# Optimization experiments

Hardware: AMD Instinct MI355X
Metric: run time of the kernel (lower is better)

## Reference

```python
import jax, jax.numpy as jnp
import numpy as np

B, T, N, D = 2, 10, 1024, 1024
NH = 16
HD = D // NH


def setup_inputs() -> dict:
    key = jax.random.key(0)
    ks = jax.random.split(key, 9)
    data = jax.random.normal(ks[0], (B, N, D), jnp.float32)
    traj_pos = jax.random.normal(ks[1], (B, T, N, 3), jnp.float32)
    q = jax.random.normal(ks[2], (B, T, N, 4), jnp.float32)
    traj_quat = q / (jnp.linalg.norm(q, axis=-1, keepdims=True) + 1e-10)
    certainty = jax.random.uniform(ks[3], (B, N), jnp.float32)
    s = 1.0 / np.sqrt(D).astype(np.float32)
    Wq = jax.random.normal(ks[4], (D, D), jnp.float32) * s
    Wk = jax.random.normal(ks[5], (D, D), jnp.float32) * s
    Wv = jax.random.normal(ks[6], (D, D), jnp.float32) * s
    Wo = jax.random.normal(ks[7], (D, D), jnp.float32) * s
    z = jnp.zeros((D,), jnp.float32)
    return {"data": data, "traj_pos": traj_pos, "traj_quat": traj_quat,
            "certainty": certainty, "Wq": Wq, "bq": z, "Wk": Wk, "bk": z,
            "Wv": Wv, "bv": z, "Wo": Wo, "bo": z}


def reference(data, traj_pos, traj_quat, certainty, Wq, bq, Wk, bk, Wv, bv, Wo, bo):
    b, n, d = data.shape
    # --- trajectory similarity scores (same for all batches: torch.mean over batch+time) ---
    # pos_dist[i,j] = mean_{b,t} ||p_bti - p_btj||
    pd = jnp.linalg.norm(traj_pos[:, :, :, None, :] - traj_pos[:, :, None, :, :], axis=-1).mean(axis=(0, 1))  # (n,n)
    qdm = jnp.linalg.norm(traj_quat[:, :, :, None, :] - traj_quat[:, :, None, :, :], axis=-1).mean(axis=(0, 1))
    qdp = jnp.linalg.norm(traj_quat[:, :, :, None, :] + traj_quat[:, :, None, :, :], axis=-1).mean(axis=(0, 1))
    qd = jnp.minimum(qdm, qdp)
    traj = jnp.exp(-pd - qd)
    traj = traj / traj.sum(axis=-1, keepdims=True)  # (n,n) row-normalized

    def proj(x, W, bias):
        return (x @ W.T + bias).reshape(b, n, NH, HD).transpose(0, 2, 1, 3)  # (b,h,n,hd)

    Q = proj(data, Wq, bq)
    K = proj(data, Wk, bk)
    V = proj(data, Wv, bv)
    scores = jnp.einsum('bhid,bhjd->bhij', Q, K) / np.sqrt(HD).astype(np.float32)
    combined = scores + 0.5 * traj[None, None]  # broadcast over (batch, heads)
    attn = jax.nn.softmax(combined, axis=-1)
    out = jnp.einsum('bhij,bhjd->bhid', attn, V).transpose(0, 2, 1, 3).reshape(b, n, d)
    out = out @ Wo.T + bo
    # certainty update from attention entropy
    avg_attn = attn.mean(axis=1)  # (b,n,n)
    p = jnp.clip(avg_attn, 1e-10, None)
    Hent = -jnp.sum(p * jnp.log(p), axis=-1)  # (b,n)
    H_max = np.log(n).astype(np.float32)
    new_certainty = jnp.maximum(certainty, jax.nn.sigmoid(H_max - Hent))
    return out, new_certainty
```

## Files before the change

kernel.cpp:

```cpp
#include <hip/hip_runtime.h>
#include <math.h>

#define NB 2
#define NN 1024
#define DD 1024
#define NHH 16
#define HDD 64
#define BTT 20

typedef unsigned short u16;
typedef short bf16x8 __attribute__((ext_vector_type(8)));
typedef float f32x4 __attribute__((ext_vector_type(4)));

#define HMAXL 6.93147180559945f
#define C1 0.18033688011112042f
#define TLC 0.72134752044448170f
#define KC  0.072134752044448170f

#define TRAJ_OFF 0
#define TL_OFF    1048576
#define DATAB_OFF 1572864
#define WQB_OFF   2621440
#define WKB_OFF   3145728
#define WVB_OFF   3670016
#define WOB_OFF   4194304
#define QB_OFF    4718592
#define KB_OFF    5767168
#define VT_OFF    6815744
#define AOB_OFF   7864320
#define LV_OFF    8912896
#define HACC_OFF  8945664
#define RS_OFF    8947712

__device__ __forceinline__ float b2f(u16 h) { return __uint_as_float(((unsigned)h) << 16); }
__device__ __forceinline__ u16 f2bf(float f) {
  unsigned u = __float_as_uint(f);
  return (u16)((u + 0x7fffu + ((u >> 16) & 1u)) >> 16);
}
__device__ __forceinline__ void dma16(const void* g, void* l) {
  __builtin_amdgcn_global_load_lds((const __attribute__((address_space(1))) void*)g,
                                   (__attribute__((address_space(3))) void*)l, 16, 0, 0);
}

__global__ __launch_bounds__(256) void conv_data_kernel(const float* __restrict__ src,
                                                        u16* __restrict__ dst) {
  int i = (blockIdx.x * 256 + threadIdx.x) * 4;
  float4 v = *(const float4*)(src + i);
  ushort4 o = {f2bf(v.x), f2bf(v.y), f2bf(v.z), f2bf(v.w)};
  *(ushort4*)(dst + i) = o;
}

__global__ __launch_bounds__(256) void conv_w_kernel(const float* __restrict__ w0,
                                                     const float* __restrict__ w1,
                                                     const float* __restrict__ w2,
                                                     const float* __restrict__ w3,
                                                     u16* __restrict__ d0, u16* __restrict__ d1,
                                                     u16* __restrict__ d2, u16* __restrict__ d3) {
  int z = blockIdx.y;
  const float* s = z == 0 ? w0 : (z == 1 ? w1 : (z == 2 ? w2 : w3));
  u16* d = z == 0 ? d0 : (z == 1 ? d1 : (z == 2 ? d2 : d3));
  int i = (blockIdx.x * 256 + threadIdx.x) * 4;
  float4 v = *(const float4*)(s + i);
  ushort4 o = {f2bf(v.x), f2bf(v.y), f2bf(v.z), f2bf(v.w)};
  *(ushort4*)(d + i) = o;
}

__global__ __launch_bounds__(256) void trajA_kernel(const float* __restrict__ pos,
                                                    const float* __restrict__ quat,
                                                    float* __restrict__ w,
                                                    float* __restrict__ rs) {
  const int tid = threadIdx.x;
  const int j = blockIdx.x * 256 + tid;
  const int i0 = blockIdx.y * 8;
  __shared__ float ld[8][BTT][8];
  if (tid < 8 * BTT) {
    int ii = tid / BTT, bt = tid % BTT;
    const float* pp = pos + ((size_t)bt * NN + i0 + ii) * 3;
    ld[ii][bt][0] = pp[0]; ld[ii][bt][1] = pp[1]; ld[ii][bt][2] = pp[2];
    *(float4*)&ld[ii][bt][4] = *(const float4*)(quat + ((size_t)bt * NN + i0 + ii) * 4);
  }
  __syncthreads();
  float acc[8] = {};
  for (int bt = 0; bt < BTT; ++bt) {
    const float* pj = pos + ((size_t)bt * NN + j) * 3;
    float pjx = pj[0], pjy = pj[1], pjz = pj[2];
    float4 qj = *(const float4*)(quat + ((size_t)bt * NN + j) * 4);
#pragma unroll
    for (int ii = 0; ii < 8; ++ii) {
      float4 pi = *(const float4*)&ld[ii][bt][0];
      float4 qi = *(const float4*)&ld[ii][bt][4];
      float dx = pi.x - pjx, dy = pi.y - pjy, dz = pi.z - pjz;
      float d2 = fmaf(dz, dz, fmaf(dy, dy, dx * dx));
      float dot = fmaf(qi.w, qj.w, fmaf(qi.z, qj.z, fmaf(qi.y, qj.y, qi.x * qj.x)));
      float t = fmaf(-2.f, fabsf(dot), 2.f);
      acc[ii] += sqrtf(d2) + sqrtf(fmaxf(t, 0.f));
    }
  }
#pragma unroll
  for (int ii = 0; ii < 8; ++ii) {
    float v = exp2f(-acc[ii] * KC);
    w[(size_t)(i0 + ii) * NN + j] = v;
    float s = v;
#pragma unroll
    for (int off = 1; off < 64; off <<= 1) s += __shfl_xor(s, off, 64);
    if ((tid & 63) == 0) atomicAdd(&rs[i0 + ii], s);
  }
}

__global__ __launch_bounds__(256) void trajB_kernel(const float* __restrict__ w,
                                                    const float* __restrict__ rs,
                                                    u16* __restrict__ tl) {
  const int i = blockIdx.x;
  const int tid = threadIdx.x;
  float inv = TLC / rs[i];
  float4 w4 = *(const float4*)(w + (size_t)i * NN + tid * 4);
  ushort4 o = {f2bf(w4.x * inv), f2bf(w4.y * inv), f2bf(w4.z * inv), f2bf(w4.w * inv)};
  *(ushort4*)(tl + (size_t)i * NN + tid * 4) = o;
}

__global__ __launch_bounds__(256) void gemm_qkv_kernel(const u16* __restrict__ Ab,
                                                       const u16* __restrict__ Wq,
                                                       const u16* __restrict__ Wk,
                                                       const u16* __restrict__ Wv,
                                                       const float* __restrict__ bq,
                                                       const float* __restrict__ bk,
                                                       const float* __restrict__ bv,
                                                       u16* __restrict__ Qb,
                                                       u16* __restrict__ Kb,
                                                       u16* __restrict__ VtT) {
  const int z = blockIdx.z;
  const u16* Wb = z == 0 ? Wq : (z == 1 ? Wk : Wv);
  const float* bias = z == 0 ? bq : (z == 1 ? bk : bv);
  __shared__ __align__(16) u16 As[128 * 32];
  __shared__ __align__(16) u16 Ws[64 * 32];
  const int tid = threadIdx.x;
  const int w = tid >> 6, l = tid & 63, g = l >> 4, ln = l & 15;
  const int bm = blockIdx.y << 7, bn = blockIdx.x << 6;
  const int rowA0 = w * 32 + (l >> 2), rowA1 = rowA0 + 16;
  const int colA = (l & 3) * 8;
  const int rowB = w * 16 + (l >> 2);
  const u16* Aptr0 = Ab + (size_t)(bm + rowA0) * DD + colA;
  const u16* Aptr1 = Ab + (size_t)(bm + rowA1) * DD + colA;
  const u16* Bptr = Wb + (size_t)(bn + rowB) * DD + colA;
  u16* ldsA0 = As + (w * 2) * 512;
  u16* ldsA1 = As + (w * 2 + 1) * 512;
  u16* ldsB = Ws + w * 512;
  f32x4 zero4 = {0.f, 0.f, 0.f, 0.f};
  f32x4 acc[4][2];
#pragma unroll
  for (int mt = 0; mt < 4; ++mt) { acc[mt][0] = zero4; acc[mt][1] = zero4; }
  const int mlo = (w & 1) * 64, nlo = (w >> 1) * 32;
  for (int k0 = 0; k0 < DD; k0 += 32) {
    __syncthreads();
    dma16(Aptr0 + k0, ldsA0);
    dma16(Aptr1 + k0, ldsA1);
    dma16(Bptr + k0, ldsB);
    __syncthreads();
    bf16x8 bfr[2];
#pragma unroll
    for (int nt = 0; nt < 2; ++nt)
      bfr[nt] = *(const bf16x8*)&Ws[(nlo + nt * 16 + ln) * 32 + g * 8];
#pragma unroll
    for (int mt = 0; mt < 4; ++mt) {
      bf16x8 af = *(const bf16x8*)&As[(mlo + mt * 16 + ln) * 32 + g * 8];
#pragma unroll
      for (int nt = 0; nt < 2; ++nt)
        acc[mt][nt] = __builtin_amdgcn_mfma_f32_16x16x32_bf16(af, bfr[nt], acc[mt][nt], 0, 0, 0);
    }
  }
#pragma unroll
  for (int nt = 0; nt < 2; ++nt) {
    int n = bn + nlo + nt * 16 + ln;
    float bb = bias[n];
    if (z == 2) {
      int row = (((bm >> 10) << 4) + (n >> 6)) * 64 + (n & 63);
#pragma unroll
      for (int mt = 0; mt < 4; ++mt) {
        int tok = ((bm & 1023) + mlo + mt * 16 + g * 4);
        ushort4 pk = {f2bf(acc[mt][nt][0] + bb), f2bf(acc[mt][nt][1] + bb),
                      f2bf(acc[mt][nt][2] + bb), f2bf(acc[mt][nt][3] + bb)};
        *(ushort4*)(VtT + (size_t)row * NN + tok) = pk;
      }
    } else {
      u16* outp = z == 0 ? Qb : Kb;
#pragma unroll
      for (int mt = 0; mt < 4; ++mt) {
#pragma unroll
        for (int r = 0; r < 4; ++r) {
          int m = bm + mlo + mt * 16 + g * 4 + r;
          outp[(size_t)m * DD + n] = f2bf(acc[mt][nt][r] + bb);
        }
      }
    }
  }
}

__global__ __launch_bounds__(256) void gemm_o_kernel(const u16* __restrict__ Ab,
                                                     const u16* __restrict__ Wb,
                                                     const float* __restrict__ bias,
                                                     float* __restrict__ C) {
  __shared__ __align__(16) u16 As[128 * 32];
  __shared__ __align__(16) u16 Ws[64 * 32];
  const int tid = threadIdx.x;
  const int w = tid >> 6, l = tid & 63, g = l >> 4, ln = l & 15;
  const int bm = blockIdx.y << 7, bn = blockIdx.x << 6;
  const int rowA0 = w * 32 + (l >> 2), rowA1 = rowA0 + 16;
  const int colA = (l & 3) * 8;
  const int rowB = w * 16 + (l >> 2);
  const u16* Aptr0 = Ab + (size_t)(bm + rowA0) * DD + colA;
  const u16* Aptr1 = Ab + (size_t)(bm + rowA1) * DD + colA;
  const u16* Bptr = Wb + (size_t)(bn + rowB) * DD + colA;
  u16* ldsA0 = As + (w * 2) * 512;
  u16* ldsA1 = As + (w * 2 + 1) * 512;
  u16* ldsB = Ws + w * 512;
  f32x4 zero4 = {0.f, 0.f, 0.f, 0.f};
  f32x4 acc[4][2];
#pragma unroll
  for (int mt = 0; mt < 4; ++mt) { acc[mt][0] = zero4; acc[mt][1] = zero4; }
  const int mlo = (w & 1) * 64, nlo = (w >> 1) * 32;
  for (int k0 = 0; k0 < DD; k0 += 32) {
    __syncthreads();
    dma16(Aptr0 + k0, ldsA0);
    dma16(Aptr1 + k0, ldsA1);
    dma16(Bptr + k0, ldsB);
    __syncthreads();
    bf16x8 bfr[2];
#pragma unroll
    for (int nt = 0; nt < 2; ++nt)
      bfr[nt] = *(const bf16x8*)&Ws[(nlo + nt * 16 + ln) * 32 + g * 8];
#pragma unroll
    for (int mt = 0; mt < 4; ++mt) {
      bf16x8 af = *(const bf16x8*)&As[(mlo + mt * 16 + ln) * 32 + g * 8];
#pragma unroll
      for (int nt = 0; nt < 2; ++nt)
        acc[mt][nt] = __builtin_amdgcn_mfma_f32_16x16x32_bf16(af, bfr[nt], acc[mt][nt], 0, 0, 0);
    }
  }
#pragma unroll
  for (int nt = 0; nt < 2; ++nt) {
    int n = bn + nlo + nt * 16 + ln;
    float bb = bias[n];
#pragma unroll
    for (int mt = 0; mt < 4; ++mt) {
#pragma unroll
      for (int r = 0; r < 4; ++r) {
        int m = bm + mlo + mt * 16 + g * 4 + r;
        C[(size_t)m * DD + n] = acc[mt][nt][r] + bb;
      }
    }
  }
}

__global__ __launch_bounds__(256) void att_kernel(const u16* __restrict__ Qb,
                                                  const u16* __restrict__ Kb,
                                                  const u16* __restrict__ VtT,
                                                  const u16* __restrict__ tl,
                                                  u16* __restrict__ AOb,
                                                  float* __restrict__ Lv) {
  const int tid = threadIdx.x;
  const int bh = blockIdx.y;
  const int b = bh >> 4, h = bh & 15;
  const int i0 = blockIdx.x << 6;
  const int w = tid >> 6, l = tid & 63, g = l >> 4, ln = l & 15;
  const int wi0 = w * 16;
  __shared__ __align__(16) u16 Qs[64 * 64];
  __shared__ __align__(16) u16 Ks[64 * 64];
  __shared__ __align__(16) u16 Vts[64 * 64];
  __shared__ __align__(16) u16 Pt[64 * 72];
  __shared__ float lsc[64];
  const int drow0 = w * 16 + (l >> 3), drow1 = drow0 + 8;
  const int dcol = (l & 7) * 8;
  dma16(Qb + ((size_t)(b * NN) + i0 + drow0) * DD + h * HDD + dcol, Qs + (w * 2) * 512);
  dma16(Qb + ((size_t)(b * NN) + i0 + drow1) * DD + h * HDD + dcol, Qs + (w * 2 + 1) * 512);
  const int ig = i0 + wi0 + ln;
  f32x4 zero4 = {0.f, 0.f, 0.f, 0.f};
  f32x4 oacc[4];
#pragma unroll
  for (int nt = 0; nt < 4; ++nt) oacc[nt] = zero4;
  float lacc = 0.f;
  for (int j0 = 0; j0 < NN; j0 += 64) {
    __syncthreads();
    dma16(Kb + ((size_t)(b * NN) + j0 + drow0) * DD + h * HDD + dcol, Ks + (w * 2) * 512);
    dma16(Kb + ((size_t)(b * NN) + j0 + drow1) * DD + h * HDD + dcol, Ks + (w * 2 + 1) * 512);
    dma16(VtT + ((size_t)(bh * 64) + drow0) * NN + j0 + dcol, Vts + (w * 2) * 512);
    dma16(VtT + ((size_t)(bh * 64) + drow1) * NN + j0 + dcol, Vts + (w * 2 + 1) * 512);
    ushort4 tlv[4];
#pragma unroll
    for (int jt = 0; jt < 4; ++jt)
      tlv[jt] = *(const ushort4*)(tl + (size_t)ig * NN + j0 + jt * 16 + g * 4);
    __syncthreads();
    bf16x8 qf[2];
    qf[0] = *(const bf16x8*)&Qs[(wi0 + ln) * 64 + g * 8];
    qf[1] = *(const bf16x8*)&Qs[(wi0 + ln) * 64 + 32 + g * 8];
    f32x4 sacc[4];
#pragma unroll
    for (int jt = 0; jt < 4; ++jt) {
      sacc[jt] = zero4;
#pragma unroll
      for (int kc = 0; kc < 2; ++kc) {
        bf16x8 af = *(const bf16x8*)&Ks[(jt * 16 + ln) * 64 + kc * 32 + g * 8];
        sacc[jt] = __builtin_amdgcn_mfma_f32_16x16x32_bf16(af, qf[kc], sacc[jt], 0, 0, 0);
      }
    }
#pragma unroll
    for (int jt = 0; jt < 4; ++jt) {
      float e0 = exp2f(sacc[jt][0] * C1 + b2f(tlv[jt].x));
      float e1 = exp2f(sacc[jt][1] * C1 + b2f(tlv[jt].y));
      float e2 = exp2f(sacc[jt][2] * C1 + b2f(tlv[jt].z));
      float e3 = exp2f(sacc[jt][3] * C1 + b2f(tlv[jt].w));
      lacc += (e0 + e1) + (e2 + e3);
      ushort4 pk = {f2bf(e0), f2bf(e1), f2bf(e2), f2bf(e3)};
      *(ushort4*)(Pt + (wi0 + ln) * 72 + jt * 16 + g * 4) = pk;
    }
    __syncthreads();
    bf16x8 pf[2];
    pf[0] = *(const bf16x8*)&Pt[(wi0 + ln) * 72 + g * 8];
    pf[1] = *(const bf16x8*)&Pt[(wi0 + ln) * 72 + 32 + g * 8];
#pragma unroll
    for (int nt = 0; nt < 4; ++nt) {
#pragma unroll
      for (int kc = 0; kc < 2; ++kc) {
        bf16x8 vf = *(const bf16x8*)&Vts[(nt * 16 + ln) * 64 + kc * 32 + g * 8];
        oacc[nt] = __builtin_amdgcn_mfma_f32_16x16x32_bf16(pf[kc], vf, oacc[nt], 0, 0, 0);
      }
    }
  }
  lacc += __shfl_xor(lacc, 16, 64);
  lacc += __shfl_xor(lacc, 32, 64);
  if (g == 0) {
    Lv[(size_t)bh * NN + i0 + wi0 + ln] = lacc;
    lsc[wi0 + ln] = 1.f / lacc;
  }
  __syncthreads();
#pragma unroll
  for (int nt = 0; nt < 4; ++nt) {
    int d = nt * 16 + ln;
#pragma unroll
    for (int r = 0; r < 4; ++r) {
      int i = wi0 + g * 4 + r;
      float v = oacc[nt][r] * lsc[i];
      AOb[((size_t)(b * NN) + i0 + i) * DD + h * HDD + d] = f2bf(v);
    }
  }
}

__global__ __launch_bounds__(256) void ent_kernel(const u16* __restrict__ Qb,
                                                  const u16* __restrict__ Kb,
                                                  const u16* __restrict__ tl,
                                                  const float* __restrict__ Lv,
                                                  float* __restrict__ Hacc) {
  const int tid = threadIdx.x;
  const int j0 = blockIdx.x << 6;
  const int i0 = blockIdx.y << 6;
  const int b = blockIdx.z;
  const int w = tid >> 6, l = tid & 63, g = l >> 4, ln = l & 15;
  const int wi0 = w * 16;
  __shared__ __align__(16) u16 Qs[64 * 64];
  __shared__ __align__(16) u16 Ks[64 * 64];
  __shared__ float linv[NHH][64];
#pragma unroll
  for (int rep = 0; rep < 4; ++rep) {
    int idx = tid + (rep << 8);
    int hh = idx >> 6, ii = idx & 63;
    linv[hh][ii] = 1.f / Lv[((size_t)((b << 4) + hh)) * NN + i0 + ii];
  }
  const int drow0 = w * 16 + (l >> 3), drow1 = drow0 + 8;
  const int dcol = (l & 7) * 8;
  const int ig = i0 + wi0 + ln;
  ushort4 tlv[4];
#pragma unroll
  for (int jt = 0; jt < 4; ++jt)
    tlv[jt] = *(const ushort4*)(tl + (size_t)ig * NN + j0 + jt * 16 + g * 4);
  float P[4][4] = {};
  f32x4 zero4 = {0.f, 0.f, 0.f, 0.f};
  for (int h = 0; h < NHH; ++h) {
    __syncthreads();
    dma16(Qb + ((size_t)(b * NN) + i0 + drow0) * DD + h * HDD + dcol, Qs + (w * 2) * 512);
    dma16(Qb + ((size_t)(b * NN) + i0 + drow1) * DD + h * HDD + dcol, Qs + (w * 2 + 1) * 512);
    dma16(Kb + ((size_t)(b * NN) + j0 + drow0) * DD + h * HDD + dcol, Ks + (w * 2) * 512);
    dma16(Kb + ((size_t)(b * NN) + j0 + drow1) * DD + h * HDD + dcol, Ks + (w * 2 + 1) * 512);
    __syncthreads();
    float li = linv[h][wi0 + ln];
    bf16x8 qf[2];
    qf[0] = *(const bf16x8*)&Qs[(wi0 + ln) * 64 + g * 8];
    qf[1] = *(const bf16x8*)&Qs[(wi0 + ln) * 64 + 32 + g * 8];
#pragma unroll
    for (int jt = 0; jt < 4; ++jt) {
      f32x4 sacc = zero4;
#pragma unroll
      for (int kc = 0; kc < 2; ++kc) {
        bf16x8 af = *(const bf16x8*)&Ks[(jt * 16 + ln) * 64 + kc * 32 + g * 8];
        sacc = __builtin_amdgcn_mfma_f32_16x16x32_bf16(af, qf[kc], sacc, 0, 0, 0);
      }
      P[jt][0] += exp2f(sacc[0] * C1 + b2f(tlv[jt].x)) * li;
      P[jt][1] += exp2f(sacc[1] * C1 + b2f(tlv[jt].y)) * li;
      P[jt][2] += exp2f(sacc[2] * C1 + b2f(tlv[jt].z)) * li;
      P[jt][3] += exp2f(sacc[3] * C1 + b2f(tlv[jt].w)) * li;
    }
  }
  float hs = 0.f;
#pragma unroll
  for (int jt = 0; jt < 4; ++jt) {
#pragma unroll
    for (int r = 0; r < 4; ++r) {
      float p = fmaxf(P[jt][r] * (1.f / NHH), 1e-10f);
      hs -= p * logf(p);
    }
  }
  hs += __shfl_xor(hs, 16, 64);
  hs += __shfl_xor(hs, 32, 64);
  if (g == 0) atomicAdd(&Hacc[(size_t)b * NN + i0 + wi0 + ln], hs);
}

__global__ __launch_bounds__(256) void zero_acc_kernel(float* __restrict__ p) {
  p[blockIdx.x * 256 + threadIdx.x] = 0.f;
}

__global__ __launch_bounds__(256) void cert_kernel(const float* __restrict__ Hacc,
                                                   const float* __restrict__ cert,
                                                   float* __restrict__ outc) {
  int idx = blockIdx.x * 256 + threadIdx.x;
  float H = Hacc[idx];
  float sg = 1.f / (1.f + expf(H - HMAXL));
  outc[idx] = fmaxf(cert[idx], sg);
}

extern "C" void kernel_launch(void* const* d_in, const int* in_sizes, int n_in,
                              void* d_out, int out_size, void* d_ws, size_t ws_size,
                              hipStream_t stream) {
  const float* data      = (const float*)d_in[0];
  const float* traj_pos  = (const float*)d_in[1];
  const float* traj_quat = (const float*)d_in[2];
  const float* certainty = (const float*)d_in[3];
  const float* Wq = (const float*)d_in[4];
  const float* bq = (const float*)d_in[5];
  const float* Wk = (const float*)d_in[6];
  const float* bk = (const float*)d_in[7];
  const float* Wv = (const float*)d_in[8];
  const float* bv = (const float*)d_in[9];
  const float* Wo = (const float*)d_in[10];
  const float* bo = (const float*)d_in[11];

  float* ws = (float*)d_ws;
  float* wtr  = ws + TRAJ_OFF;
  u16* tl    = (u16*)(ws + TL_OFF);
  u16* datab = (u16*)(ws + DATAB_OFF);
  u16* wqb   = (u16*)(ws + WQB_OFF);
  u16* wkb   = (u16*)(ws + WKB_OFF);
  u16* wvb   = (u16*)(ws + WVB_OFF);
  u16* wob   = (u16*)(ws + WOB_OFF);
  u16* Qb    = (u16*)(ws + QB_OFF);
  u16* Kb    = (u16*)(ws + KB_OFF);
  u16* VtT   = (u16*)(ws + VT_OFF);
  u16* AOb   = (u16*)(ws + AOB_OFF);
  float* Lv   = ws + LV_OFF;
  float* Hacc = ws + HACC_OFF;
  float* rs   = ws + RS_OFF;
  float* out  = (float*)d_out;
  float* outc = out + (size_t)NB * NN * DD;

  zero_acc_kernel<<<12, 256, 0, stream>>>(Hacc);
  conv_data_kernel<<<2048, 256, 0, stream>>>(data, datab);
  conv_w_kernel<<<dim3(1024, 4), 256, 0, stream>>>(Wq, Wk, Wv, Wo, wqb, wkb, wvb, wob);
  trajA_kernel<<<dim3(4, 128), 256, 0, stream>>>(traj_pos, traj_quat, wtr, rs);
  trajB_kernel<<<NN, 256, 0, stream>>>(wtr, rs, tl);
  gemm_qkv_kernel<<<dim3(16, 16, 3), 256, 0, stream>>>(datab, wqb, wkb, wvb, bq, bk, bv,
                                                       Qb, Kb, VtT);
  att_kernel<<<dim3(NN / 64, NB * NHH), 256, 0, stream>>>(Qb, Kb, VtT, tl, AOb, Lv);
  ent_kernel<<<dim3(NN / 64, NN / 64, NB), 256, 0, stream>>>(Qb, Kb, tl, Lv, Hacc);
  cert_kernel<<<(NB * NN) / 256, 256, 0, stream>>>(Hacc, certainty, outc);
  gemm_o_kernel<<<dim3(16, 16), 256, 0, stream>>>(AOb, wob, bo, out);
}
```

Before: 232.2 us.

## Enlarge GEMM tiles, batch attention/entropy key loads, merge conversion kernels

```diff
diff --git a/kernel.cpp b/kernel.cpp
--- a/kernel.cpp
+++ b/kernel.cpp
@@ -42,24 +42,24 @@
                                    (__attribute__((address_space(3))) void*)l, 16, 0, 0);
 }
 
-__global__ __launch_bounds__(256) void conv_data_kernel(const float* __restrict__ src,
-                                                        u16* __restrict__ dst) {
-  int i = (blockIdx.x * 256 + threadIdx.x) * 4;
-  float4 v = *(const float4*)(src + i);
-  ushort4 o = {f2bf(v.x), f2bf(v.y), f2bf(v.z), f2bf(v.w)};
-  *(ushort4*)(dst + i) = o;
-}
-
-__global__ __launch_bounds__(256) void conv_w_kernel(const float* __restrict__ w0,
-                                                     const float* __restrict__ w1,
-                                                     const float* __restrict__ w2,
-                                                     const float* __restrict__ w3,
-                                                     u16* __restrict__ d0, u16* __restrict__ d1,
-                                                     u16* __restrict__ d2, u16* __restrict__ d3) {
+__global__ __launch_bounds__(256) void conv_kernel(const float* __restrict__ data,
+                                                   const float* __restrict__ w0,
+                                                   const float* __restrict__ w1,
+                                                   const float* __restrict__ w2,
+                                                   const float* __restrict__ w3,
+                                                   u16* __restrict__ dd,
+                                                   u16* __restrict__ d0, u16* __restrict__ d1,
+                                                   u16* __restrict__ d2, u16* __restrict__ d3) {
   int z = blockIdx.y;
-  const float* s = z == 0 ? w0 : (z == 1 ? w1 : (z == 2 ? w2 : w3));
-  u16* d = z == 0 ? d0 : (z == 1 ? d1 : (z == 2 ? d2 : d3));
-  int i = (blockIdx.x * 256 + threadIdx.x) * 4;
+  const float* s;
+  u16* d;
+  size_t off = 0;
+  if (z < 2) { s = data; d = dd; off = (size_t)z * 1048576; }
+  else if (z == 2) { s = w0; d = d0; }
+  else if (z == 3) { s = w1; d = d1; }
+  else if (z == 4) { s = w2; d = d2; }
+  else { s = w3; d = d3; }
+  size_t i = off + (size_t)(blockIdx.x * 256 + threadIdx.x) * 4;
   float4 v = *(const float4*)(s + i);
   ushort4 o = {f2bf(v.x), f2bf(v.y), f2bf(v.z), f2bf(v.w)};
   *(ushort4*)(d + i) = o;
@@ -132,51 +132,54 @@
   const u16* Wb = z == 0 ? Wq : (z == 1 ? Wk : Wv);
   const float* bias = z == 0 ? bq : (z == 1 ? bk : bv);
   __shared__ __align__(16) u16 As[128 * 32];
-  __shared__ __align__(16) u16 Ws[64 * 32];
+  __shared__ __align__(16) u16 Bs[128 * 32];
   const int tid = threadIdx.x;
   const int w = tid >> 6, l = tid & 63, g = l >> 4, ln = l & 15;
-  const int bm = blockIdx.y << 7, bn = blockIdx.x << 6;
-  const int rowA0 = w * 32 + (l >> 2), rowA1 = rowA0 + 16;
-  const int colA = (l & 3) * 8;
-  const int rowB = w * 16 + (l >> 2);
-  const u16* Aptr0 = Ab + (size_t)(bm + rowA0) * DD + colA;
-  const u16* Aptr1 = Ab + (size_t)(bm + rowA1) * DD + colA;
-  const u16* Bptr = Wb + (size_t)(bn + rowB) * DD + colA;
-  u16* ldsA0 = As + (w * 2) * 512;
-  u16* ldsA1 = As + (w * 2 + 1) * 512;
-  u16* ldsB = Ws + w * 512;
+  const int bm = blockIdx.y << 7, bn = blockIdx.x << 7;
+  const int srow = w * 16 + (l >> 2);
+  const int scol = (l & 3) * 8;
+  const u16* Ap0 = Ab + (size_t)(bm + srow) * DD + scol;
+  const u16* Ap1 = Ab + (size_t)(bm + 64 + srow) * DD + scol;
+  const u16* Bp0 = Wb + (size_t)(bn + srow) * DD + scol;
+  const u16* Bp1 = Wb + (size_t)(bn + 64 + srow) * DD + scol;
+  u16* dA0 = As + w * 512;
+  u16* dA1 = As + 2048 + w * 512;
+  u16* dB0 = Bs + w * 512;
+  u16* dB1 = Bs + 2048 + w * 512;
+  const int mw = (w & 1) * 64, nw = (w >> 1) * 64;
   f32x4 zero4 = {0.f, 0.f, 0.f, 0.f};
-  f32x4 acc[4][2];
-#pragma unroll
-  for (int mt = 0; mt < 4; ++mt) { acc[mt][0] = zero4; acc[mt][1] = zero4; }
-  const int mlo = (w & 1) * 64, nlo = (w >> 1) * 32;
+  f32x4 acc[4][4];
+#pragma unroll
+  for (int mt = 0; mt < 4; ++mt)
+#pragma unroll
+    for (int nt = 0; nt < 4; ++nt) acc[mt][nt] = zero4;
   for (int k0 = 0; k0 < DD; k0 += 32) {
     __syncthreads();
-    dma16(Aptr0 + k0, ldsA0);
-    dma16(Aptr1 + k0, ldsA1);
-    dma16(Bptr + k0, ldsB);
-    __syncthreads();
-    bf16x8 bfr[2];
-#pragma unroll
-    for (int nt = 0; nt < 2; ++nt)
-      bfr[nt] = *(const bf16x8*)&Ws[(nlo + nt * 16 + ln) * 32 + g * 8];
-#pragma unroll
-    for (int mt = 0; mt < 4; ++mt) {
-      bf16x8 af = *(const bf16x8*)&As[(mlo + mt * 16 + ln) * 32 + g * 8];
-#pragma unroll
-      for (int nt = 0; nt < 2; ++nt)
-        acc[mt][nt] = __builtin_amdgcn_mfma_f32_16x16x32_bf16(af, bfr[nt], acc[mt][nt], 0, 0, 0);
-    }
-  }
-#pragma unroll
-  for (int nt = 0; nt < 2; ++nt) {
-    int n = bn + nlo + nt * 16 + ln;
+    dma16(Ap0 + k0, dA0); dma16(Ap1 + k0, dA1);
+    dma16(Bp0 + k0, dB0); dma16(Bp1 + k0, dB1);
+    __syncthreads();
+    bf16x8 bfr[4], afr[4];
+#pragma unroll
+    for (int nt = 0; nt < 4; ++nt)
+      bfr[nt] = *(const bf16x8*)&Bs[(nw + nt * 16 + ln) * 32 + g * 8];
+#pragma unroll
+    for (int mt = 0; mt < 4; ++mt)
+      afr[mt] = *(const bf16x8*)&As[(mw + mt * 16 + ln) * 32 + g * 8];
+#pragma unroll
+    for (int mt = 0; mt < 4; ++mt)
+#pragma unroll
+      for (int nt = 0; nt < 4; ++nt)
+        acc[mt][nt] = __builtin_amdgcn_mfma_f32_16x16x32_bf16(afr[mt], bfr[nt], acc[mt][nt], 0, 0, 0);
+  }
+#pragma unroll
+  for (int nt = 0; nt < 4; ++nt) {
+    int n = bn + nw + nt * 16 + ln;
     float bb = bias[n];
     if (z == 2) {
       int row = (((bm >> 10) << 4) + (n >> 6)) * 64 + (n & 63);
 #pragma unroll
       for (int mt = 0; mt < 4; ++mt) {
-        int tok = ((bm & 1023) + mlo + mt * 16 + g * 4);
+        int tok = (bm & 1023) + mw + mt * 16 + g * 4;
         ushort4 pk = {f2bf(acc[mt][nt][0] + bb), f2bf(acc[mt][nt][1] + bb),
                       f2bf(acc[mt][nt][2] + bb), f2bf(acc[mt][nt][3] + bb)};
         *(ushort4*)(VtT + (size_t)row * NN + tok) = pk;
@@ -187,7 +190,7 @@
       for (int mt = 0; mt < 4; ++mt) {
 #pragma unroll
         for (int r = 0; r < 4; ++r) {
-          int m = bm + mlo + mt * 16 + g * 4 + r;
+          int m = bm + mw + mt * 16 + g * 4 + r;
           outp[(size_t)m * DD + n] = f2bf(acc[mt][nt][r] + bb);
         }
       }
@@ -200,51 +203,54 @@
                                                      const float* __restrict__ bias,
                                                      float* __restrict__ C) {
   __shared__ __align__(16) u16 As[128 * 32];
-  __shared__ __align__(16) u16 Ws[64 * 32];
+  __shared__ __align__(16) u16 Bs[128 * 32];
   const int tid = threadIdx.x;
   const int w = tid >> 6, l = tid & 63, g = l >> 4, ln = l & 15;
-  const int bm = blockIdx.y << 7, bn = blockIdx.x << 6;
-  const int rowA0 = w * 32 + (l >> 2), rowA1 = rowA0 + 16;
-  const int colA = (l & 3) * 8;
-  const int rowB = w * 16 + (l >> 2);
-  const u16* Aptr0 = Ab + (size_t)(bm + rowA0) * DD + colA;
-  const u16* Aptr1 = Ab + (size_t)(bm + rowA1) * DD + colA;
-  const u16* Bptr = Wb + (size_t)(bn + rowB) * DD + colA;
-  u16* ldsA0 = As + (w * 2) * 512;
-  u16* ldsA1 = As + (w * 2 + 1) * 512;
-  u16* ldsB = Ws + w * 512;
+  const int bm = blockIdx.y << 7, bn = blockIdx.x << 7;
+  const int srow = w * 16 + (l >> 2);
+  const int scol = (l & 3) * 8;
+  const u16* Ap0 = Ab + (size_t)(bm + srow) * DD + scol;
+  const u16* Ap1 = Ab + (size_t)(bm + 64 + srow) * DD + scol;
+  const u16* Bp0 = Wb + (size_t)(bn + srow) * DD + scol;
+  const u16* Bp1 = Wb + (size_t)(bn + 64 + srow) * DD + scol;
+  u16* dA0 = As + w * 512;
+  u16* dA1 = As + 2048 + w * 512;
+  u16* dB0 = Bs + w * 512;
+  u16* dB1 = Bs + 2048 + w * 512;
+  const int mw = (w & 1) * 64, nw = (w >> 1) * 64;
   f32x4 zero4 = {0.f, 0.f, 0.f, 0.f};
-  f32x4 acc[4][2];
-#pragma unroll
-  for (int mt = 0; mt < 4; ++mt) { acc[mt][0] = zero4; acc[mt][1] = zero4; }
-  const int mlo = (w & 1) * 64, nlo = (w >> 1) * 32;
+  f32x4 acc[4][4];
+#pragma unroll
+  for (int mt = 0; mt < 4; ++mt)
+#pragma unroll
+    for (int nt = 0; nt < 4; ++nt) acc[mt][nt] = zero4;
   for (int k0 = 0; k0 < DD; k0 += 32) {
     __syncthreads();
-    dma16(Aptr0 + k0, ldsA0);
-    dma16(Aptr1 + k0, ldsA1);
-    dma16(Bptr + k0, ldsB);
-    __syncthreads();
-    bf16x8 bfr[2];
-#pragma unroll
-    for (int nt = 0; nt < 2; ++nt)
-      bfr[nt] = *(const bf16x8*)&Ws[(nlo + nt * 16 + ln) * 32 + g * 8];
+    dma16(Ap0 + k0, dA0); dma16(Ap1 + k0, dA1);
+    dma16(Bp0 + k0, dB0); dma16(Bp1 + k0, dB1);
+    __syncthreads();
+    bf16x8 bfr[4], afr[4];
+#pragma unroll
+    for (int nt = 0; nt < 4; ++nt)
+      bfr[nt] = *(const bf16x8*)&Bs[(nw + nt * 16 + ln) * 32 + g * 8];
+#pragma unroll
+    for (int mt = 0; mt < 4; ++mt)
+      afr[mt] = *(const bf16x8*)&As[(mw + mt * 16 + ln) * 32 + g * 8];
+#pragma unroll
+    for (int mt = 0; mt < 4; ++mt)
+#pragma unroll
+      for (int nt = 0; nt < 4; ++nt)
+        acc[mt][nt] = __builtin_amdgcn_mfma_f32_16x16x32_bf16(afr[mt], bfr[nt], acc[mt][nt], 0, 0, 0);
+  }
+#pragma unroll
+  for (int nt = 0; nt < 4; ++nt) {
+    int n = bn + nw + nt * 16 + ln;
+    float bb = bias[n];
 #pragma unroll
     for (int mt = 0; mt < 4; ++mt) {
-      bf16x8 af = *(const bf16x8*)&As[(mlo + mt * 16 + ln) * 32 + g * 8];
-#pragma unroll
-      for (int nt = 0; nt < 2; ++nt)
-        acc[mt][nt] = __builtin_amdgcn_mfma_f32_16x16x32_bf16(af, bfr[nt], acc[mt][nt], 0, 0, 0);
-    }
-  }
-#pragma unroll
-  for (int nt = 0; nt < 2; ++nt) {
-    int n = bn + nlo + nt * 16 + ln;
-    float bb = bias[n];
-#pragma unroll
-    for (int mt = 0; mt < 4; ++mt) {
 #pragma unroll
       for (int r = 0; r < 4; ++r) {
-        int m = bm + mlo + mt * 16 + g * 4 + r;
+        int m = bm + mw + mt * 16 + g * 4 + r;
         C[(size_t)m * DD + n] = acc[mt][nt][r] + bb;
       }
     }
@@ -264,8 +270,8 @@
   const int w = tid >> 6, l = tid & 63, g = l >> 4, ln = l & 15;
   const int wi0 = w * 16;
   __shared__ __align__(16) u16 Qs[64 * 64];
-  __shared__ __align__(16) u16 Ks[64 * 64];
-  __shared__ __align__(16) u16 Vts[64 * 64];
+  __shared__ __align__(16) u16 Ks[2][64 * 64];
+  __shared__ __align__(16) u16 Vts[2][64 * 64];
   __shared__ __align__(16) u16 Pt[64 * 72];
   __shared__ float lsc[64];
   const int drow0 = w * 16 + (l >> 3), drow1 = drow0 + 8;
@@ -278,50 +284,58 @@
 #pragma unroll
   for (int nt = 0; nt < 4; ++nt) oacc[nt] = zero4;
   float lacc = 0.f;
-  for (int j0 = 0; j0 < NN; j0 += 64) {
-    __syncthreads();
-    dma16(Kb + ((size_t)(b * NN) + j0 + drow0) * DD + h * HDD + dcol, Ks + (w * 2) * 512);
-    dma16(Kb + ((size_t)(b * NN) + j0 + drow1) * DD + h * HDD + dcol, Ks + (w * 2 + 1) * 512);
-    dma16(VtT + ((size_t)(bh * 64) + drow0) * NN + j0 + dcol, Vts + (w * 2) * 512);
-    dma16(VtT + ((size_t)(bh * 64) + drow1) * NN + j0 + dcol, Vts + (w * 2 + 1) * 512);
-    ushort4 tlv[4];
-#pragma unroll
-    for (int jt = 0; jt < 4; ++jt)
-      tlv[jt] = *(const ushort4*)(tl + (size_t)ig * NN + j0 + jt * 16 + g * 4);
+  for (int j0 = 0; j0 < NN; j0 += 128) {
+    __syncthreads();
+#pragma unroll
+    for (int u = 0; u < 2; ++u) {
+      int jb = j0 + u * 64;
+      dma16(Kb + ((size_t)(b * NN) + jb + drow0) * DD + h * HDD + dcol, Ks[u] + (w * 2) * 512);
+      dma16(Kb + ((size_t)(b * NN) + jb + drow1) * DD + h * HDD + dcol, Ks[u] + (w * 2 + 1) * 512);
+      dma16(VtT + ((size_t)(bh * 64) + drow0) * NN + jb + dcol, Vts[u] + (w * 2) * 512);
+      dma16(VtT + ((size_t)(bh * 64) + drow1) * NN + jb + dcol, Vts[u] + (w * 2 + 1) * 512);
+    }
+    ushort4 tlv[2][4];
+#pragma unroll
+    for (int u = 0; u < 2; ++u)
+#pragma unroll
+      for (int jt = 0; jt < 4; ++jt)
+        tlv[u][jt] = *(const ushort4*)(tl + (size_t)ig * NN + j0 + u * 64 + jt * 16 + g * 4);
     __syncthreads();
     bf16x8 qf[2];
     qf[0] = *(const bf16x8*)&Qs[(wi0 + ln) * 64 + g * 8];
     qf[1] = *(const bf16x8*)&Qs[(wi0 + ln) * 64 + 32 + g * 8];
-    f32x4 sacc[4];
-#pragma unroll
-    for (int jt = 0; jt < 4; ++jt) {
-      sacc[jt] = zero4;
-#pragma unroll
-      for (int kc = 0; kc < 2; ++kc) {
-        bf16x8 af = *(const bf16x8*)&Ks[(jt * 16 + ln) * 64 + kc * 32 + g * 8];
-        sacc[jt] = __builtin_amdgcn_mfma_f32_16x16x32_bf16(af, qf[kc], sacc[jt], 0, 0, 0);
-      }
-    }
-#pragma unroll
-    for (int jt = 0; jt < 4; ++jt) {
-      float e0 = exp2f(sacc[jt][0] * C1 + b2f(tlv[jt].x));
-      float e1 = exp2f(sacc[jt][1] * C1 + b2f(tlv[jt].y));
-      float e2 = exp2f(sacc[jt][2] * C1 + b2f(tlv[jt].z));
-      float e3 = exp2f(sacc[jt][3] * C1 + b2f(tlv[jt].w));
-      lacc += (e0 + e1) + (e2 + e3);
-      ushort4 pk = {f2bf(e0), f2bf(e1), f2bf(e2), f2bf(e3)};
-      *(ushort4*)(Pt + (wi0 + ln) * 72 + jt * 16 + g * 4) = pk;
-    }
-    __syncthreads();
-    bf16x8 pf[2];
-    pf[0] = *(const bf16x8*)&Pt[(wi0 + ln) * 72 + g * 8];
-    pf[1] = *(const bf16x8*)&Pt[(wi0 + ln) * 72 + 32 + g * 8];
-#pragma unroll
-    for (int nt = 0; nt < 4; ++nt) {
-#pragma unroll
-      for (int kc = 0; kc < 2; ++kc) {
-        bf16x8 vf = *(const bf16x8*)&Vts[(nt * 16 + ln) * 64 + kc * 32 + g * 8];
-        oacc[nt] = __builtin_amdgcn_mfma_f32_16x16x32_bf16(pf[kc], vf, oacc[nt], 0, 0, 0);
+#pragma unroll
+    for (int u = 0; u < 2; ++u) {
+      f32x4 sacc[4];
+#pragma unroll
+      for (int jt = 0; jt < 4; ++jt) {
+        sacc[jt] = zero4;
+#pragma unroll
+        for (int kc = 0; kc < 2; ++kc) {
+          bf16x8 af = *(const bf16x8*)&Ks[u][(jt * 16 + ln) * 64 + kc * 32 + g * 8];
+          sacc[jt] = __builtin_amdgcn_mfma_f32_16x16x32_bf16(af, qf[kc], sacc[jt], 0, 0, 0);
+        }
+      }
+#pragma unroll
+      for (int jt = 0; jt < 4; ++jt) {
+        float e0 = exp2f(sacc[jt][0] * C1 + b2f(tlv[u][jt].x));
+        float e1 = exp2f(sacc[jt][1] * C1 + b2f(tlv[u][jt].y));
+        float e2 = exp2f(sacc[jt][2] * C1 + b2f(tlv[u][jt].z));
+        float e3 = exp2f(sacc[jt][3] * C1 + b2f(tlv[u][jt].w));
+        lacc += (e0 + e1) + (e2 + e3);
+        ushort4 pk = {f2bf(e0), f2bf(e1), f2bf(e2), f2bf(e3)};
+        *(ushort4*)(Pt + (wi0 + ln) * 72 + jt * 16 + g * 4) = pk;
+      }
+      bf16x8 pf[2];
+      pf[0] = *(const bf16x8*)&Pt[(wi0 + ln) * 72 + g * 8];
+      pf[1] = *(const bf16x8*)&Pt[(wi0 + ln) * 72 + 32 + g * 8];
+#pragma unroll
+      for (int nt = 0; nt < 4; ++nt) {
+#pragma unroll
+        for (int kc = 0; kc < 2; ++kc) {
+          bf16x8 vf = *(const bf16x8*)&Vts[u][(nt * 16 + ln) * 64 + kc * 32 + g * 8];
+          oacc[nt] = __builtin_amdgcn_mfma_f32_16x16x32_bf16(pf[kc], vf, oacc[nt], 0, 0, 0);
+        }
       }
     }
   }
@@ -355,8 +369,8 @@
   const int b = blockIdx.z;
   const int w = tid >> 6, l = tid & 63, g = l >> 4, ln = l & 15;
   const int wi0 = w * 16;
-  __shared__ __align__(16) u16 Qs[64 * 64];
-  __shared__ __align__(16) u16 Ks[64 * 64];
+  __shared__ __align__(16) u16 Qs[64 * 256];
+  __shared__ __align__(16) u16 Ks[64 * 256];
   __shared__ float linv[NHH][64];
 #pragma unroll
   for (int rep = 0; rep < 4; ++rep) {
@@ -364,8 +378,10 @@
     int hh = idx >> 6, ii = idx & 63;
     linv[hh][ii] = 1.f / Lv[((size_t)((b << 4) + hh)) * NN + i0 + ii];
   }
-  const int drow0 = w * 16 + (l >> 3), drow1 = drow0 + 8;
-  const int dcol = (l & 7) * 8;
+  const int srow = w * 2 + (l >> 5);
+  const int scol = (l & 31) * 8;
+  const u16* Qg = Qb + ((size_t)(b * NN) + i0 + srow) * DD + scol;
+  const u16* Kg = Kb + ((size_t)(b * NN) + j0 + srow) * DD + scol;
   const int ig = i0 + wi0 + ln;
   ushort4 tlv[4];
 #pragma unroll
@@ -373,29 +389,33 @@
     tlv[jt] = *(const ushort4*)(tl + (size_t)ig * NN + j0 + jt * 16 + g * 4);
   float P[4][4] = {};
   f32x4 zero4 = {0.f, 0.f, 0.f, 0.f};
-  for (int h = 0; h < NHH; ++h) {
-    __syncthreads();
-    dma16(Qb + ((size_t)(b * NN) + i0 + drow0) * DD + h * HDD + dcol, Qs + (w * 2) * 512);
-    dma16(Qb + ((size_t)(b * NN) + i0 + drow1) * DD + h * HDD + dcol, Qs + (w * 2 + 1) * 512);
-    dma16(Kb + ((size_t)(b * NN) + j0 + drow0) * DD + h * HDD + dcol, Ks + (w * 2) * 512);
-    dma16(Kb + ((size_t)(b * NN) + j0 + drow1) * DD + h * HDD + dcol, Ks + (w * 2 + 1) * 512);
-    __syncthreads();
-    float li = linv[h][wi0 + ln];
-    bf16x8 qf[2];
-    qf[0] = *(const bf16x8*)&Qs[(wi0 + ln) * 64 + g * 8];
-    qf[1] = *(const bf16x8*)&Qs[(wi0 + ln) * 64 + 32 + g * 8];
-#pragma unroll
-    for (int jt = 0; jt < 4; ++jt) {
-      f32x4 sacc = zero4;
-#pragma unroll
-      for (int kc = 0; kc < 2; ++kc) {
-        bf16x8 af = *(const bf16x8*)&Ks[(jt * 16 + ln) * 64 + kc * 32 + g * 8];
-        sacc = __builtin_amdgcn_mfma_f32_16x16x32_bf16(af, qf[kc], sacc, 0, 0, 0);
-      }
-      P[jt][0] += exp2f(sacc[0] * C1 + b2f(tlv[jt].x)) * li;
-      P[jt][1] += exp2f(sacc[1] * C1 + b2f(tlv[jt].y)) * li;
-      P[jt][2] += exp2f(sacc[2] * C1 + b2f(tlv[jt].z)) * li;
-      P[jt][3] += exp2f(sacc[3] * C1 + b2f(tlv[jt].w)) * li;
+  for (int hb = 0; hb < 4; ++hb) {
+    __syncthreads();
+#pragma unroll
+    for (int c = 0; c < 8; ++c) {
+      dma16(Qg + (size_t)(c * 8) * DD + hb * 256, Qs + (c * 8 + w * 2) * 256);
+      dma16(Kg + (size_t)(c * 8) * DD + hb * 256, Ks + (c * 8 + w * 2) * 256);
+    }
+    __syncthreads();
+#pragma unroll
+    for (int hl = 0; hl < 4; ++hl) {
+      float li = linv[hb * 4 + hl][wi0 + ln];
+      bf16x8 qf[2];
+      qf[0] = *(const bf16x8*)&Qs[(wi0 + ln) * 256 + hl * 64 + g * 8];
+      qf[1] = *(const bf16x8*)&Qs[(wi0 + ln) * 256 + hl * 64 + 32 + g * 8];
+#pragma unroll
+      for (int jt = 0; jt < 4; ++jt) {
+        f32x4 sacc = zero4;
+#pragma unroll
+        for (int kc = 0; kc < 2; ++kc) {
+          bf16x8 af = *(const bf16x8*)&Ks[(jt * 16 + ln) * 256 + hl * 64 + kc * 32 + g * 8];
+          sacc = __builtin_amdgcn_mfma_f32_16x16x32_bf16(af, qf[kc], sacc, 0, 0, 0);
+        }
+        P[jt][0] += exp2f(sacc[0] * C1 + b2f(tlv[jt].x)) * li;
+        P[jt][1] += exp2f(sacc[1] * C1 + b2f(tlv[jt].y)) * li;
+        P[jt][2] += exp2f(sacc[2] * C1 + b2f(tlv[jt].z)) * li;
+        P[jt][3] += exp2f(sacc[3] * C1 + b2f(tlv[jt].w)) * li;
+      }
     }
   }
   float hs = 0.f;
@@ -460,14 +480,14 @@
   float* outc = out + (size_t)NB * NN * DD;
 
   zero_acc_kernel<<<12, 256, 0, stream>>>(Hacc);
-  conv_data_kernel<<<2048, 256, 0, stream>>>(data, datab);
-  conv_w_kernel<<<dim3(1024, 4), 256, 0, stream>>>(Wq, Wk, Wv, Wo, wqb, wkb, wvb, wob);
+  conv_kernel<<<dim3(1024, 6), 256, 0, stream>>>(data, Wq, Wk, Wv, Wo,
+                                                 datab, wqb, wkb, wvb, wob);
   trajA_kernel<<<dim3(4, 128), 256, 0, stream>>>(traj_pos, traj_quat, wtr, rs);
   trajB_kernel<<<NN, 256, 0, stream>>>(wtr, rs, tl);
-  gemm_qkv_kernel<<<dim3(16, 16, 3), 256, 0, stream>>>(datab, wqb, wkb, wvb, bq, bk, bv,
-                                                       Qb, Kb, VtT);
+  gemm_qkv_kernel<<<dim3(8, 16, 3), 256, 0, stream>>>(datab, wqb, wkb, wvb, bq, bk, bv,
+                                                      Qb, Kb, VtT);
   att_kernel<<<dim3(NN / 64, NB * NHH), 256, 0, stream>>>(Qb, Kb, VtT, tl, AOb, Lv);
   ent_kernel<<<dim3(NN / 64, NN / 64, NB), 256, 0, stream>>>(Qb, Kb, tl, Lv, Hacc);
   cert_kernel<<<(NB * NN) / 256, 256, 0, stream>>>(Hacc, certainty, outc);
-  gemm_o_kernel<<<dim3(16, 16), 256, 0, stream>>>(AOb, wob, bo, out);
-}
+  gemm_o_kernel<<<dim3(8, 16), 256, 0, stream>>>(AOb, wob, bo, out);
+}
```

Result: slower. 237.5 us (+2.3%).
